# Performance work log

Measured on AMD Instinct MI355X. Metric: run time of the kernel, lower is better.

## Reference

```python
import jax, jax.numpy as jnp
from jax import lax
import numpy as np

B, H, W_, C, F = 4, 32, 32, 16, 16
KH, KW = 3, 3
L = 1.0


def setup_inputs() -> dict:
    key = jax.random.key(0)
    k1, k2, k3, k4 = jax.random.split(key, 4)
    inputs = jax.random.normal(k1, (B, H, W_, C), dtype=jnp.float32)
    # lecun_normal-style scales (stddev = 1/sqrt(fan_in))
    m_scale = 1.0 / np.sqrt(H * W_ * 1)
    g_scale = 1.0 / np.sqrt(KH * KW * C)
    M = jax.random.normal(k2, (H, W_, 1, H, W_, 1), dtype=jnp.float32) * m_scale
    Wp = jax.random.normal(k3, (H, W_, 1, H, W_, 1), dtype=jnp.float32) * m_scale
    G = jax.random.normal(k4, (H, W_, KH, KW, C, F), dtype=jnp.float32) * g_scale
    return {"inputs": inputs, "M": M, "Wp": Wp, "G": G}


def reference(inputs, M, Wp, G):
    b, h, w, c = inputs.shape
    kh, kw, f = G.shape[2], G.shape[3], G.shape[5]
    M2 = M[:, :, 0, :, :, 0]   # (i,j,p,q)
    W2 = Wp[:, :, 0, :, :, 0]  # (i,j,p,q)
    # first_term[b,i,j,c] = sum_pq M[i,j,p,q] * inputs[b,p,q,c]
    first = jnp.einsum('ijpq,bpqc->bijc', M2, inputs)
    # One big conv: kernel (kh,kw,c, h*w*f) gives shifted for every output pixel (i,j)
    K = jnp.transpose(G, (2, 3, 4, 0, 1, 5)).reshape(kh, kw, c, h * w * f)
    shifted = lax.conv_general_dilated(
        inputs, K, window_strides=(1, 1), padding='SAME',
        dimension_numbers=('NHWC', 'HWIO', 'NHWC'))
    shifted = shifted.reshape(b, h, w, h, w, f)  # (b,p,q,i,j,f)
    diff = jax.nn.relu(inputs[:, :, :, None, None, :] - shifted)  # (b,p,q,i,j,c)
    # second_term[b,i,j,c] = sum_pq W[i,j,p,q] * relu(inputs - shifted)[b,p,q,i,j,c]
    second = jnp.einsum('ijpq,bpqijc->bijc', W2, diff)
    return first - L * second
```

## Files before the change

kernel.cpp:

```cpp
#include <hip/hip_runtime.h>


typedef __attribute__((ext_vector_type(8))) short bf16x8;
typedef __attribute__((ext_vector_type(4))) float f32x4;

__device__ inline unsigned short f2bf(float x) {
    unsigned u = __float_as_uint(x);
    u += 0x7FFFu + ((u >> 16) & 1u);
    return (unsigned short)(u >> 16);
}
__device__ inline unsigned pack2(float a, float b) {
    return (unsigned)f2bf(a) | ((unsigned)f2bf(b) << 16);
}

__global__ __launch_bounds__(256) void build_A(const float* __restrict__ inp,
                                               uint4* __restrict__ A) {
    const int row = blockIdx.x * 256 + threadIdx.x;
    const int b = row >> 10, pq = row & 1023;
    const int p = pq >> 5, q = pq & 31;
    const int tile = row >> 4, m = row & 15;
    const float* inb = inp + b * 16384;

#pragma unroll
    for (int tap = 0; tap < 9; ++tap) {
        const int dh = tap / 3, dw = tap % 3;
        const int pp = p + dh - 1, qq = q + dw - 1;
        const bool v = ((unsigned)pp < 32u) && ((unsigned)qq < 32u);
        uint4 lo = {0, 0, 0, 0}, hi = {0, 0, 0, 0};
        if (v) {
            const float4* s = (const float4*)(inb + (pp * 32 + qq) * 16);
            float4 f0 = s[0], f1 = s[1], f2 = s[2], f3 = s[3];
            lo.x = pack2(f0.x, f0.y); lo.y = pack2(f0.z, f0.w);
            lo.z = pack2(f1.x, f1.y); lo.w = pack2(f1.z, f1.w);
            hi.x = pack2(f2.x, f2.y); hi.y = pack2(f2.z, f2.w);
            hi.z = pack2(f3.x, f3.y); hi.w = pack2(f3.z, f3.w);
        }
        const int kk = tap >> 1, qa = (tap & 1) * 2;
        const int base = (tile * 5 + kk) * 64 + qa * 16 + m;
        A[base] = lo;
        A[base + 16] = hi;
    }
    const uint4 z = {0, 0, 0, 0};
    const int base = (tile * 5 + 4) * 64 + 2 * 16 + m;
    A[base] = z;
    A[base + 16] = z;
}

__global__ __launch_bounds__(512, 2) void inrf_main(
    const float* __restrict__ inp,
    const float* __restrict__ M,
    const float* __restrict__ Wp,
    const float* __restrict__ G,
    const uint4* __restrict__ Aw,
    float* __restrict__ out)
{
    const int bid = blockIdx.x;
    const int t = threadIdx.x;

    __shared__ __align__(16) float W2l[4096];
    __shared__ __align__(16) float M2l[4096];
    __shared__ __align__(16) float G_l[9216];
    __shared__ float red[8][64];

    {
        const float* Wg = Wp + bid * 4096;
        const float* Mg = M  + bid * 4096;
        for (int i = t; i < 4096; i += 512) { W2l[i] = Wg[i]; M2l[i] = Mg[i]; }
        const float* Gg = G + bid * 9216;
        for (int i = t; i < 9216; i += 512) G_l[i] = Gg[i];
    }
    __syncthreads();

    const int l = t & 63, w = t >> 6;
    const int quad = l >> 4, col = l & 15;
    const int b = w >> 1;

    bf16x8 Bf[4][5];
#pragma unroll
    for (int ij = 0; ij < 4; ++ij) {
#pragma unroll
        for (int kk = 0; kk < 5; ++kk) {
            bf16x8 f;
#pragma unroll
            for (int j = 0; j < 8; ++j) {
                const int k = kk * 32 + quad * 8 + j;
                const float v = (k < 144) ? G_l[ij * 2304 + k * 16 + col] : 0.f;
                f[j] = (short)f2bf(v);
            }
            Bf[ij][kk] = f;
        }
    }

    float accv[4] = {0.f, 0.f, 0.f, 0.f};
    const int tile0 = b * 64 + (w & 1) * 32;
    const float* inb = inp + b * 16384;

    uint4 Acur[5], Anxt[5];
    float vcur[4], vnxt[4];
    {
        const int tg = tile0;
#pragma unroll
        for (int kk = 0; kk < 5; ++kk) Acur[kk] = Aw[(tg * 5 + kk) * 64 + l];
        const int pqb = (tg & 63) * 16 + quad * 4;
#pragma unroll
        for (int r = 0; r < 4; ++r) vcur[r] = inb[(pqb + r) * 16 + col];
    }

    for (int i = 0; i < 32; ++i) {
        const int tg = tile0 + i;
        if (i < 31) {
            const int tn = tg + 1;
#pragma unroll
            for (int kk = 0; kk < 5; ++kk) Anxt[kk] = Aw[(tn * 5 + kk) * 64 + l];
            const int pqb = (tn & 63) * 16 + quad * 4;
#pragma unroll
            for (int r = 0; r < 4; ++r) vnxt[r] = inb[(pqb + r) * 16 + col];
        }

        f32x4 C[4];
#pragma unroll
        for (int ij = 0; ij < 4; ++ij) C[ij] = (f32x4){0.f, 0.f, 0.f, 0.f};
#pragma unroll
        for (int kk = 0; kk < 5; ++kk) {
            const bf16x8 a = __builtin_bit_cast(bf16x8, Acur[kk]);
#pragma unroll
            for (int ij = 0; ij < 4; ++ij)
                C[ij] = __builtin_amdgcn_mfma_f32_16x16x32_bf16(a, Bf[ij][kk], C[ij], 0, 0, 0);
        }

        const int pqb = (tg & 63) * 16 + quad * 4;
#pragma unroll
        for (int ij = 0; ij < 4; ++ij) {
            const float4 w2 = *(const float4*)&W2l[ij * 1024 + pqb];
            const float4 m2 = *(const float4*)&M2l[ij * 1024 + pqb];
            accv[ij] += m2.x * vcur[0] - w2.x * fmaxf(vcur[0] - C[ij][0], 0.f);
            accv[ij] += m2.y * vcur[1] - w2.y * fmaxf(vcur[1] - C[ij][1], 0.f);
            accv[ij] += m2.z * vcur[2] - w2.z * fmaxf(vcur[2] - C[ij][2], 0.f);
            accv[ij] += m2.w * vcur[3] - w2.w * fmaxf(vcur[3] - C[ij][3], 0.f);
        }

#pragma unroll
        for (int kk = 0; kk < 5; ++kk) Acur[kk] = Anxt[kk];
#pragma unroll
        for (int r = 0; r < 4; ++r) vcur[r] = vnxt[r];
    }

#pragma unroll
    for (int ij = 0; ij < 4; ++ij) {
        float v = accv[ij];
        v += __shfl_xor(v, 16);
        v += __shfl_xor(v, 32);
        if (l < 16) red[w][ij * 16 + l] = v;
    }
    __syncthreads();

    if (t < 256) {
        const int ob = t >> 6, oij = (t >> 4) & 3, oc = t & 15;
        const float r0 = red[ob * 2][oij * 16 + oc] + red[ob * 2 + 1][oij * 16 + oc];
        out[ob * 16384 + (bid * 4 + oij) * 16 + oc] = r0;
    }
}

extern "C" void kernel_launch(void* const* d_in, const int* in_sizes, int n_in,
                              void* d_out, int out_size, void* d_ws, size_t ws_size,
                              hipStream_t stream) {
    const float* inp = (const float*)d_in[0];
    const float* M   = (const float*)d_in[1];
    const float* Wp  = (const float*)d_in[2];
    const float* G   = (const float*)d_in[3];
    float* out = (float*)d_out;

    uint4* A = (uint4*)d_ws;
    build_A<<<dim3(16), dim3(256), 0, stream>>>(inp, A);
    inrf_main<<<dim3(256), dim3(512), 0, stream>>>(inp, M, Wp, G, A, out);
}
```

Measured before the change: 103.0 us.

## Parallelize A-build across taps, prepack fp32 inputs, load G directly, double-buffer loop

The A-matrix build now uses one thread per (tap, half, row) across 320 or 384 blocks instead of 16 blocks looping over taps, which raises parallelism in the prep kernel. An optional pre-packed float4 copy of the inputs in MFMA-fragment order replaces four strided scalar loads per tile with one vector load. G is read straight from global memory into the B fragments, which removes the 36 KB LDS staging and one barrier and shrinks LDS use. The main loop is manually double-buffered with explicit A0/A1 register sets instead of copying next into current. The cost is extra workspace, a larger prep kernel and higher register pressure.

```diff
diff --git a/kernel.cpp b/kernel.cpp
--- a/kernel.cpp
+++ b/kernel.cpp
@@ -13,45 +13,57 @@
     return (unsigned)f2bf(a) | ((unsigned)f2bf(b) << 16);
 }
 
+template<bool XF>
 __global__ __launch_bounds__(256) void build_A(const float* __restrict__ inp,
-                                               uint4* __restrict__ A) {
-    const int row = blockIdx.x * 256 + threadIdx.x;
+                                               uint4* __restrict__ A,
+                                               float4* __restrict__ Xf) {
+    const int tid = blockIdx.x * 256 + threadIdx.x;
+    const int u = tid >> 12;
+    if (XF && u >= 20) {
+        const int idx = tid - 81920;
+        const int tile = idx >> 6;
+        const int ll = idx & 63;
+        const int rowb = tile * 16 + (ll >> 4) * 4;
+        const int col = ll & 15;
+        float4 v;
+        v.x = inp[(rowb + 0) * 16 + col];
+        v.y = inp[(rowb + 1) * 16 + col];
+        v.z = inp[(rowb + 2) * 16 + col];
+        v.w = inp[(rowb + 3) * 16 + col];
+        Xf[idx] = v;
+        return;
+    }
+    const int row = tid & 4095;
+    const int tile = row >> 4, m = row & 15;
+    if (u >= 18) {
+        const uint4 z = {0, 0, 0, 0};
+        A[(tile * 5 + 4) * 64 + (u - 16) * 16 + m] = z;
+        return;
+    }
+    const int tap = u >> 1, h = u & 1;
+    const int dh = tap / 3, dw = tap - dh * 3;
     const int b = row >> 10, pq = row & 1023;
     const int p = pq >> 5, q = pq & 31;
-    const int tile = row >> 4, m = row & 15;
-    const float* inb = inp + b * 16384;
-
-#pragma unroll
-    for (int tap = 0; tap < 9; ++tap) {
-        const int dh = tap / 3, dw = tap % 3;
-        const int pp = p + dh - 1, qq = q + dw - 1;
-        const bool v = ((unsigned)pp < 32u) && ((unsigned)qq < 32u);
-        uint4 lo = {0, 0, 0, 0}, hi = {0, 0, 0, 0};
-        if (v) {
-            const float4* s = (const float4*)(inb + (pp * 32 + qq) * 16);
-            float4 f0 = s[0], f1 = s[1], f2 = s[2], f3 = s[3];
-            lo.x = pack2(f0.x, f0.y); lo.y = pack2(f0.z, f0.w);
-            lo.z = pack2(f1.x, f1.y); lo.w = pack2(f1.z, f1.w);
-            hi.x = pack2(f2.x, f2.y); hi.y = pack2(f2.z, f2.w);
-            hi.z = pack2(f3.x, f3.y); hi.w = pack2(f3.z, f3.w);
-        }
-        const int kk = tap >> 1, qa = (tap & 1) * 2;
-        const int base = (tile * 5 + kk) * 64 + qa * 16 + m;
-        A[base] = lo;
-        A[base + 16] = hi;
-    }
-    const uint4 z = {0, 0, 0, 0};
-    const int base = (tile * 5 + 4) * 64 + 2 * 16 + m;
-    A[base] = z;
-    A[base + 16] = z;
-}
-
+    const int pp = p + dh - 1, qq = q + dw - 1;
+    const int kk = tap >> 1, quad = (tap & 1) * 2 + h;
+    uint4 o = {0, 0, 0, 0};
+    if (((unsigned)pp < 32u) && ((unsigned)qq < 32u)) {
+        const float4* s = (const float4*)(inp + b * 16384 + (pp * 32 + qq) * 16 + 8 * h);
+        const float4 f0 = s[0], f1 = s[1];
+        o.x = pack2(f0.x, f0.y); o.y = pack2(f0.z, f0.w);
+        o.z = pack2(f1.x, f1.y); o.w = pack2(f1.z, f1.w);
+    }
+    A[(tile * 5 + kk) * 64 + quad * 16 + m] = o;
+}
+
+template<bool XF>
 __global__ __launch_bounds__(512, 2) void inrf_main(
     const float* __restrict__ inp,
     const float* __restrict__ M,
     const float* __restrict__ Wp,
     const float* __restrict__ G,
     const uint4* __restrict__ Aw,
+    const float4* __restrict__ Xf,
     float* __restrict__ out)
 {
     const int bid = blockIdx.x;
@@ -59,22 +71,23 @@
 
     __shared__ __align__(16) float W2l[4096];
     __shared__ __align__(16) float M2l[4096];
-    __shared__ __align__(16) float G_l[9216];
     __shared__ float red[8][64];
 
     {
         const float* Wg = Wp + bid * 4096;
         const float* Mg = M  + bid * 4096;
-        for (int i = t; i < 4096; i += 512) { W2l[i] = Wg[i]; M2l[i] = Mg[i]; }
-        const float* Gg = G + bid * 9216;
-        for (int i = t; i < 9216; i += 512) G_l[i] = Gg[i];
-    }
-    __syncthreads();
+#pragma unroll
+        for (int i = 0; i < 8; ++i) {
+            W2l[t + i * 512] = Wg[t + i * 512];
+            M2l[t + i * 512] = Mg[t + i * 512];
+        }
+    }
 
     const int l = t & 63, w = t >> 6;
     const int quad = l >> 4, col = l & 15;
     const int b = w >> 1;
 
+    const float* Gg = G + bid * 9216;
     bf16x8 Bf[4][5];
 #pragma unroll
     for (int ij = 0; ij < 4; ++ij) {
@@ -84,65 +97,68 @@
 #pragma unroll
             for (int j = 0; j < 8; ++j) {
                 const int k = kk * 32 + quad * 8 + j;
-                const float v = (k < 144) ? G_l[ij * 2304 + k * 16 + col] : 0.f;
+                const float v = (k < 144) ? Gg[ij * 2304 + k * 16 + col] : 0.f;
                 f[j] = (short)f2bf(v);
             }
             Bf[ij][kk] = f;
         }
     }
 
-    float accv[4] = {0.f, 0.f, 0.f, 0.f};
+    __syncthreads();
+
     const int tile0 = b * 64 + (w & 1) * 32;
     const float* inb = inp + b * 16384;
-
-    uint4 Acur[5], Anxt[5];
-    float vcur[4], vnxt[4];
-    {
-        const int tg = tile0;
-#pragma unroll
-        for (int kk = 0; kk < 5; ++kk) Acur[kk] = Aw[(tg * 5 + kk) * 64 + l];
-        const int pqb = (tg & 63) * 16 + quad * 4;
-#pragma unroll
-        for (int r = 0; r < 4; ++r) vcur[r] = inb[(pqb + r) * 16 + col];
-    }
-
-    for (int i = 0; i < 32; ++i) {
-        const int tg = tile0 + i;
-        if (i < 31) {
-            const int tn = tg + 1;
-#pragma unroll
-            for (int kk = 0; kk < 5; ++kk) Anxt[kk] = Aw[(tn * 5 + kk) * 64 + l];
+    (void)inb;
+
+    float accv[4] = {0.f, 0.f, 0.f, 0.f};
+
+    uint4 A0[5], A1[5];
+    float4 v0, v1;
+
+    auto prefetch = [&](uint4 (&Ar)[5], float4& vr, int tn) {
+#pragma unroll
+        for (int kk = 0; kk < 5; ++kk) Ar[kk] = Aw[(tn * 5 + kk) * 64 + l];
+        if (XF) {
+            vr = Xf[tn * 64 + l];
+        } else {
             const int pqb = (tn & 63) * 16 + quad * 4;
-#pragma unroll
-            for (int r = 0; r < 4; ++r) vnxt[r] = inb[(pqb + r) * 16 + col];
-        }
-
+            vr.x = inb[(pqb + 0) * 16 + col];
+            vr.y = inb[(pqb + 1) * 16 + col];
+            vr.z = inb[(pqb + 2) * 16 + col];
+            vr.w = inb[(pqb + 3) * 16 + col];
+        }
+    };
+
+    auto compute = [&](const uint4 (&Ar)[5], const float4& vr, int tg) {
         f32x4 C[4];
 #pragma unroll
         for (int ij = 0; ij < 4; ++ij) C[ij] = (f32x4){0.f, 0.f, 0.f, 0.f};
 #pragma unroll
         for (int kk = 0; kk < 5; ++kk) {
-            const bf16x8 a = __builtin_bit_cast(bf16x8, Acur[kk]);
+            const bf16x8 a = __builtin_bit_cast(bf16x8, Ar[kk]);
 #pragma unroll
             for (int ij = 0; ij < 4; ++ij)
                 C[ij] = __builtin_amdgcn_mfma_f32_16x16x32_bf16(a, Bf[ij][kk], C[ij], 0, 0, 0);
         }
-
         const int pqb = (tg & 63) * 16 + quad * 4;
 #pragma unroll
         for (int ij = 0; ij < 4; ++ij) {
             const float4 w2 = *(const float4*)&W2l[ij * 1024 + pqb];
             const float4 m2 = *(const float4*)&M2l[ij * 1024 + pqb];
-            accv[ij] += m2.x * vcur[0] - w2.x * fmaxf(vcur[0] - C[ij][0], 0.f);
-            accv[ij] += m2.y * vcur[1] - w2.y * fmaxf(vcur[1] - C[ij][1], 0.f);
-            accv[ij] += m2.z * vcur[2] - w2.z * fmaxf(vcur[2] - C[ij][2], 0.f);
-            accv[ij] += m2.w * vcur[3] - w2.w * fmaxf(vcur[3] - C[ij][3], 0.f);
-        }
-
-#pragma unroll
-        for (int kk = 0; kk < 5; ++kk) Acur[kk] = Anxt[kk];
-#pragma unroll
-        for (int r = 0; r < 4; ++r) vcur[r] = vnxt[r];
+            accv[ij] += m2.x * vr.x - w2.x * fmaxf(vr.x - C[ij][0], 0.f);
+            accv[ij] += m2.y * vr.y - w2.y * fmaxf(vr.y - C[ij][1], 0.f);
+            accv[ij] += m2.z * vr.z - w2.z * fmaxf(vr.z - C[ij][2], 0.f);
+            accv[ij] += m2.w * vr.w - w2.w * fmaxf(vr.w - C[ij][3], 0.f);
+        }
+    };
+
+    prefetch(A0, v0, tile0);
+#pragma unroll 1
+    for (int i = 0; i < 32; i += 2) {
+        prefetch(A1, v1, tile0 + i + 1);
+        compute(A0, v0, tile0 + i);
+        if (i + 2 < 32) prefetch(A0, v0, tile0 + i + 2);
+        compute(A1, v1, tile0 + i + 1);
     }
 
 #pragma unroll
@@ -170,7 +186,15 @@
     const float* G   = (const float*)d_in[3];
     float* out = (float*)d_out;
 
-    uint4* A = (uint4*)d_ws;
-    build_A<<<dim3(16), dim3(256), 0, stream>>>(inp, A);
-    inrf_main<<<dim3(256), dim3(512), 0, stream>>>(inp, M, Wp, G, A, out);
-}
+    uint4*  A  = (uint4*)d_ws;
+    float4* Xf = (float4*)((char*)d_ws + 81920 * sizeof(uint4));
+    const size_t need = 81920 * sizeof(uint4) + 16384 * sizeof(float4);
+
+    if (ws_size >= need) {
+        build_A<true><<<dim3(384), dim3(256), 0, stream>>>(inp, A, Xf);
+        inrf_main<true><<<dim3(256), dim3(512), 0, stream>>>(inp, M, Wp, G, A, Xf, out);
+    } else {
+        build_A<false><<<dim3(320), dim3(256), 0, stream>>>(inp, A, nullptr);
+        inrf_main<false><<<dim3(256), dim3(512), 0, stream>>>(inp, M, Wp, G, A, nullptr, out);
+    }
+}
```

New measurement: 98.31 us. -4.5%, faster.
